# Performance work log

Hardware: AMD Instinct MI355X
Metric: run time of the kernel (lower is better)

The kernel has to match this reference:

```python
import jax, jax.numpy as jnp
import numpy as np

N, E = 50000, 1600000
IN_DIM, HID, HEADS, DH, NCLS = 1280, 256, 4, 64, 6
NEG_SLOPE = 0.2
LN_EPS = 1e-5


def setup_inputs() -> dict:
    key = jax.random.key(0)
    ks = jax.random.split(key, 24)
    p = {}
    p['x'] = jax.random.normal(ks[0], (N, IN_DIM), dtype=jnp.float32)
    p['edge_index'] = jax.random.randint(ks[1], (2, E), 0, N, dtype=jnp.int64)
    s = 0.05
    p['W_in'] = jax.random.normal(ks[2], (IN_DIM, HID), dtype=jnp.float32) * s
    p['b_in'] = jnp.zeros((HID,), jnp.float32)
    for l in range(2):
        p[f'W_gat{l}'] = jax.random.normal(ks[3 + 6 * l], (HID, HEADS * DH), dtype=jnp.float32) * s
        p[f'att_src{l}'] = jax.random.normal(ks[4 + 6 * l], (HEADS, DH), dtype=jnp.float32) * s
        p[f'att_dst{l}'] = jax.random.normal(ks[5 + 6 * l], (HEADS, DH), dtype=jnp.float32) * s
        p[f'b_gat{l}'] = jnp.zeros((HEADS * DH,), jnp.float32)
        p[f'ln_g{l}'] = jnp.ones((HID,), jnp.float32)
        p[f'ln_b{l}'] = jnp.zeros((HID,), jnp.float32)
    p['W_c1'] = jax.random.normal(ks[20], (HID, HID // 2), dtype=jnp.float32) * s
    p['b_c1'] = jnp.zeros((HID // 2,), jnp.float32)
    p['W_c2'] = jax.random.normal(ks[21], (HID // 2, NCLS), dtype=jnp.float32) * s
    p['b_c2'] = jnp.zeros((NCLS,), jnp.float32)
    return p


def _layer_norm(h, g, b):
    mu = jnp.mean(h, axis=-1, keepdims=True)
    var = jnp.mean((h - mu) ** 2, axis=-1, keepdims=True)
    return (h - mu) * jax.lax.rsqrt(var + LN_EPS) * g + b


def _gat_conv(h, src, dst, W, a_src, a_dst, bias):
    # h: [N, HID] -> per-head projections [N, H, DH]
    xh = (h @ W).reshape(N, HEADS, DH)
    al_src = jnp.sum(xh * a_src, axis=-1)  # [N, H]
    al_dst = jnp.sum(xh * a_dst, axis=-1)  # [N, H]
    e = jax.nn.leaky_relu(al_src[src] + al_dst[dst], NEG_SLOPE)  # [E', H]
    # edge softmax over incoming edges of each destination node
    m = jax.ops.segment_max(e, dst, num_segments=N)
    e = jnp.exp(e - m[dst])
    denom = jax.ops.segment_sum(e, dst, num_segments=N)
    w = e / denom[dst]  # [E', H]
    msg = xh[src] * w[:, :, None]  # [E', H, DH]
    out = jax.ops.segment_sum(msg, dst, num_segments=N)  # [N, H, DH]
    return out.reshape(N, HEADS * DH) + bias


def reference(x, edge_index, W_in, b_in, W_gat0, att_src0, att_dst0, b_gat0, ln_g0, ln_b0,
              W_gat1, att_src1, att_dst1, b_gat1, ln_g1, ln_b1, W_c1, b_c1, W_c2, b_c2):
    # add self loops (PyG GATConv default)
    loop = jnp.arange(N, dtype=edge_index.dtype)
    src = jnp.concatenate([edge_index[0], loop])
    dst = jnp.concatenate([edge_index[1], loop])

    h = jax.nn.relu(x @ W_in + b_in)

    for (Wg, asrc, adst, bg, g, b) in ((W_gat0, att_src0, att_dst0, b_gat0, ln_g0, ln_b0),
                                       (W_gat1, att_src1, att_dst1, b_gat1, ln_g1, ln_b1)):
        h_new = _gat_conv(h, src, dst, Wg, asrc, adst, bg)
        h_new = jax.nn.relu(_layer_norm(h_new, g, b))
        h = h + h_new

    logits = jax.nn.relu(h @ W_c1 + b_c1) @ W_c2 + b_c2
    return logits
```

## Files before the change

### kernel.cpp

```cpp
#include <hip/hip_runtime.h>

#define NN 50000
#define EE 1600000
#define INDIM 1280
#define HID 256
#define HEADS 4
#define DHD 64
#define NCLS 6
#define NEG 0.2f
#define LNEPS 1e-5f

typedef __attribute__((ext_vector_type(8))) short short8;
typedef __attribute__((ext_vector_type(4))) float floatx4;

__device__ __forceinline__ unsigned short f2b(float f) {
    unsigned int u = __float_as_uint(f);
    u += 0x7FFF + ((u >> 16) & 1);
    return (unsigned short)(u >> 16);
}
__device__ __forceinline__ float b2f(unsigned short b) {
    return __uint_as_float(((unsigned int)b) << 16);
}

#define WAIT_LGKM0() __builtin_amdgcn_s_waitcnt(0xC07F)
#define VMCNT6() asm volatile("s_waitcnt vmcnt(6)" ::: "memory")
#define VMCNT0() asm volatile("s_waitcnt vmcnt(0)" ::: "memory")

typedef const __attribute__((address_space(1))) unsigned int g_u32;
typedef __attribute__((address_space(3))) unsigned int l_u32;
#define GLOAD16(gp, lp) __builtin_amdgcn_global_load_lds((g_u32*)(gp), (l_u32*)(lp), 16, 0, 0)

__global__ void init_cnt_kernel(int* __restrict__ cnt) {
    int n = blockIdx.x * 256 + threadIdx.x;
    if (n < NN) cnt[n] = 1;
}

__global__ void count_edges_kernel(const int* __restrict__ dst, int* __restrict__ cnt) {
    int e = blockIdx.x * 256 + threadIdx.x;
    if (e < EE) atomicAdd(&cnt[dst[e]], 1);
}

__global__ __launch_bounds__(1024) void scan1_kernel(const int* __restrict__ cnt,
                                                     int* __restrict__ scanned,
                                                     int* __restrict__ chtot, int n) {
    __shared__ int wsum[16];
    int tid = threadIdx.x, lane = tid & 63, wv = tid >> 6;
    int i = blockIdx.x * 1024 + tid;
    int s = (i < n) ? cnt[i] : 0;
#pragma unroll
    for (int off = 1; off < 64; off <<= 1) {
        int t = __shfl_up(s, off, 64);
        if (lane >= off) s += t;
    }
    if (lane == 63) wsum[wv] = s;
    __syncthreads();
    if (tid < 16) {
        int ws = wsum[tid];
#pragma unroll
        for (int off = 1; off < 16; off <<= 1) {
            int t = __shfl_up(ws, off, 16);
            if (tid >= off) ws += t;
        }
        wsum[tid] = ws;
    }
    __syncthreads();
    s += (wv > 0) ? wsum[wv - 1] : 0;
    if (i < n) scanned[i] = s;
    if (tid == 1023) chtot[blockIdx.x] = s;
}

__global__ void scan2_kernel(int* __restrict__ chtot, int nch) {
    int lane = threadIdx.x;
    int v = (lane < nch) ? chtot[lane] : 0;
#pragma unroll
    for (int off = 1; off < 64; off <<= 1) {
        int t = __shfl_up(v, off, 64);
        if (lane >= off) v += t;
    }
    if (lane < nch) chtot[lane] = v;
}

__global__ void scan3_kernel(const int* __restrict__ scanned, const int* __restrict__ chtot,
                             int* __restrict__ rowptr, int n) {
    int i = blockIdx.x * 256 + threadIdx.x;
    if (i == 0) rowptr[0] = 0;
    if (i < n) {
        int ch = i >> 10;
        rowptr[i + 1] = scanned[i] + (ch ? chtot[ch - 1] : 0);
    }
}

__global__ void copyfill_kernel(const int* __restrict__ rowptr, int* __restrict__ cursor,
                                int* __restrict__ csr) {
    int n = blockIdx.x * 256 + threadIdx.x;
    if (n < NN) {
        int p = rowptr[n];
        csr[p] = n;
        cursor[n] = p + 1;
    }
}

__global__ void scatter_edges_kernel(const int* __restrict__ src, const int* __restrict__ dst,
                                     int* __restrict__ cursor, int* __restrict__ csr) {
    int e = blockIdx.x * 256 + threadIdx.x;
    if (e < EE) {
        int d = dst[e];
        int pos = atomicAdd(&cursor[d], 1);
        csr[pos] = src[e];
    }
}

__global__ void pack_w_kernel(const float* __restrict__ W, unsigned short* __restrict__ out,
                              int K, int N) {
    int idx = blockIdx.x * 256 + threadIdx.x;
    int total = (K >> 6) * (N >> 4) * 2 * 64;
    if (idx >= total) return;
    int ln = idx & 63;
    int t = idx >> 6;
    int ks = t & 1; t >>= 1;
    int NT = N >> 4;
    int nt = t % NT, kc = t / NT;
    int n = nt * 16 + (ln & 15);
    int k = kc * 64 + ks * 32 + ((ln >> 4) << 3);
    unsigned short u[8];
#pragma unroll
    for (int j = 0; j < 8; j++) u[j] = f2b(W[(size_t)(k + j) * N + n]);
    *(int4*)&out[(size_t)idx * 8] = *(const int4*)u;
}

__global__ void pack_w32_kernel(const float* __restrict__ W, unsigned short* __restrict__ out) {
    int idx = blockIdx.x * 256 + threadIdx.x;
    if (idx >= 40 * 16 * 64) return;
    int ln = idx & 63;
    int t = idx >> 6;
    int nt = t & 15;
    int s = t >> 4;
    int n = nt * 16 + (ln & 15);
    int k = s * 32 + ((ln >> 4) << 3);
    unsigned short u[8];
#pragma unroll
    for (int j = 0; j < 8; j++) u[j] = f2b(W[(size_t)(k + j) * HID + n]);
    *(int4*)&out[(size_t)idx * 8] = *(const int4*)u;
}

__global__ __launch_bounds__(256) void inproj_kernel(const float* __restrict__ Af,
                                                     const unsigned short* __restrict__ B32,
                                                     const float* __restrict__ bias,
                                                     float* __restrict__ Cf,
                                                     unsigned short* __restrict__ Cb) {
    constexpr int KS = 40;
    constexpr int ABYTES = 8192;
    constexpr int BBYTES = 16384;
    constexpr int SBYTES = ABYTES + BBYTES;
    __shared__ __align__(16) char lds[3 * SBYTES];
    int tid = threadIdx.x, wv = tid >> 6, ln = tid & 63;
    int m0 = blockIdx.x * 64;

    int arow0 = wv * 16 + (ln >> 3);
    int arow1 = arow0 + 8;
    int acb = ((ln & 7) * 16) ^ (((ln >> 3) & 7) << 4);
    const char* asrc0 = (const char*)(Af + (size_t)min(m0 + arow0, NN - 1) * INDIM) + acb;
    const char* asrc1 = (const char*)(Af + (size_t)min(m0 + arow1, NN - 1) * INDIM) + acb;
    const char* bsrc = (const char*)B32 + wv * 4096 + ln * 16;

    int aslot = wv * 2048 + ln * 16;
    int bslot = wv * 4096 + ln * 16;

    auto issue = [&](int k) {
        char* a = &lds[(k % 3) * SBYTES];
        char* b = a + ABYTES;
        GLOAD16(asrc0 + (size_t)k * 128, a + aslot);
        GLOAD16(asrc1 + (size_t)k * 128, a + aslot + 1024);
        const char* bs = bsrc + (size_t)k * BBYTES;
        GLOAD16(bs, b + bslot);
        GLOAD16(bs + 1024, b + bslot + 1024);
        GLOAD16(bs + 2048, b + bslot + 2048);
        GLOAD16(bs + 3072, b + bslot + 3072);
    };

    floatx4 acc[4][4] = {};
    int g32 = (ln >> 4) * 32;

    issue(0);
    issue(1);

    for (int k = 0; k < KS; k++) {
        if (k == KS - 1) VMCNT0(); else VMCNT6();
        __builtin_amdgcn_s_barrier();
        asm volatile("" ::: "memory");
        if (k + 2 < KS) issue(k + 2);

        const char* a = &lds[(k % 3) * SBYTES];
        const char* b = a + ABYTES;
        short8 bfrag[4];
#pragma unroll
        for (int nw = 0; nw < 4; nw++)
            bfrag[nw] = *(const short8*)(b + (((wv * 4 + nw) * 64 + ln) << 4));
#pragma unroll
        for (int mt = 0; mt < 4; mt++) {
            int row = mt * 16 + (ln & 15);
            int base = row * 128;
            int sw = (row & 7) << 4;
            float4 f0 = *(const float4*)(a + base + (g32 ^ sw));
            float4 f1 = *(const float4*)(a + base + ((g32 + 16) ^ sw));
            union { int4 i; short8 s; } u;
            asm("v_cvt_pk_bf16_f32 %0, %1, %2" : "=v"(u.i.x) : "v"(f0.x), "v"(f0.y));
            asm("v_cvt_pk_bf16_f32 %0, %1, %2" : "=v"(u.i.y) : "v"(f0.z), "v"(f0.w));
            asm("v_cvt_pk_bf16_f32 %0, %1, %2" : "=v"(u.i.z) : "v"(f1.x), "v"(f1.y));
            asm("v_cvt_pk_bf16_f32 %0, %1, %2" : "=v"(u.i.w) : "v"(f1.z), "v"(f1.w));
#pragma unroll
            for (int nw = 0; nw < 4; nw++)
                acc[mt][nw] = __builtin_amdgcn_mfma_f32_16x16x32_bf16(
                    u.s, bfrag[nw], acc[mt][nw], 0, 0, 0);
        }
        asm volatile("" ::: "memory");
    }

#pragma unroll
    for (int mt = 0; mt < 4; mt++) {
#pragma unroll
        for (int nw = 0; nw < 4; nw++) {
            int col = (wv * 4 + nw) * 16 + (ln & 15);
            int rb = m0 + mt * 16 + (ln >> 4) * 4;
            float bi = bias[col];
#pragma unroll
            for (int r = 0; r < 4; r++) {
                int row = rb + r;
                if (row < NN) {
                    float v = fmaxf(acc[mt][nw][r] + bi, 0.f);
                    Cf[(size_t)row * HID + col] = v;
                    Cb[(size_t)row * HID + col] = f2b(v);
                }
            }
        }
    }
}

template <int KI, int NT, int ACT, int WB16, int PROJ, int CLS>
__global__ __launch_bounds__(256) void pgemm_kernel(const unsigned short* __restrict__ Ab,
                                                    const unsigned short* __restrict__ Bf,
                                                    const float* __restrict__ bias,
                                                    unsigned short* __restrict__ Cb,
                                                    const float* __restrict__ aps,
                                                    const float* __restrict__ apd,
                                                    float* __restrict__ als,
                                                    float* __restrict__ ald,
                                                    const float* __restrict__ W2,
                                                    const float* __restrict__ b2,
                                                    float* __restrict__ out2,
                                                    int M) {
    constexpr int NW = NT / 4;
    constexpr int K = KI * 64;
    __shared__ __align__(16) unsigned short Als[2][4096];
    int tid = threadIdx.x, wv = tid >> 6, ln = tid & 63;
    int m0 = blockIdx.x * 64;

    int srow[2], scol[2];
#pragma unroll
    for (int i = 0; i < 2; i++) {
        int s = tid + i * 256;
        int r = s >> 3;
        srow[i] = min(m0 + r, M - 1);
        scol[i] = ((s & 7) ^ (r & 7)) * 8;
    }

    floatx4 acc[4][NW] = {};
    short8 breg[2][NW * 2];
    int4 ai0[2], ai1[2];

    auto issueA = [&](int k, int4* ai) {
#pragma unroll
        for (int i = 0; i < 2; i++)
            ai[i] = *(const int4*)(Ab + (size_t)srow[i] * K + k * 64 + scol[i]);
    };
    auto issueB = [&](int k, short8* b) {
#pragma unroll
        for (int nw = 0; nw < NW; nw++)
#pragma unroll
            for (int ks = 0; ks < 2; ks++)
                b[nw * 2 + ks] = *(const short8*)(
                    Bf + ((((size_t)k * NT + (wv * NW + nw)) * 2 + ks) * 64 + ln) * 8);
    };
    auto writeA = [&](int k, const int4* ai) {
        unsigned short* dst = &Als[k & 1][0];
#pragma unroll
        for (int i = 0; i < 2; i++) *(int4*)&dst[(tid + i * 256) * 8] = ai[i];
    };
    auto compute = [&](int k, const short8* b) {
        const unsigned short* src = &Als[k & 1][0];
#pragma unroll
        for (int ks = 0; ks < 2; ks++) {
            short8 a[4];
#pragma unroll
            for (int mt = 0; mt < 4; mt++) {
                int row = mt * 16 + (ln & 15);
                int g = ks * 4 + (ln >> 4);
                a[mt] = *(const short8*)&src[row * 64 + (g ^ (row & 7)) * 8];
            }
#pragma unroll
            for (int nw = 0; nw < NW; nw++)
#pragma unroll
                for (int mt = 0; mt < 4; mt++)
                    acc[mt][nw] = __builtin_amdgcn_mfma_f32_16x16x32_bf16(
                        a[mt], b[nw * 2 + ks], acc[mt][nw], 0, 0, 0);
        }
    };

    issueA(0, ai0);
    issueB(0, breg[0]);
    writeA(0, ai0);
    WAIT_LGKM0();
    __builtin_amdgcn_s_barrier();

#pragma unroll
    for (int kk = 0; kk < KI / 2; kk++) {
        int k = kk * 2;
        issueA(k + 1, ai1);
        issueB(k + 1, breg[1]);
        compute(k, breg[0]);
        writeA(k + 1, ai1);
        WAIT_LGKM0();
        __builtin_amdgcn_s_barrier();
        if (k + 2 < KI) {
            issueA(k + 2, ai0);
            issueB(k + 2, breg[0]);
        }
        compute(k + 1, breg[1]);
        if (k + 2 < KI) {
            writeA(k + 2, ai0);
            WAIT_LGKM0();
            __builtin_amdgcn_s_barrier();
        }
    }

    constexpr int Nout = NT * 16;
    if constexpr (WB16) {
#pragma unroll
        for (int mt = 0; mt < 4; mt++) {
#pragma unroll
            for (int nw = 0; nw < NW; nw++) {
                int col = (wv * NW + nw) * 16 + (ln & 15);
                int rb = m0 + mt * 16 + (ln >> 4) * 4;
                float bi = bias ? bias[col] : 0.f;
#pragma unroll
                for (int r = 0; r < 4; r++) {
                    int row = rb + r;
                    if (row < M) {
                        float v = acc[mt][nw][r] + bi;
                        if (ACT) v = fmaxf(v, 0.f);
                        Cb[(size_t)row * Nout + col] = f2b(v);
                    }
                }
            }
        }
    }

    if constexpr (PROJ) {
        float avs[NW], avd[NW];
#pragma unroll
        for (int nw = 0; nw < NW; nw++) {
            int d = nw * 16 + (ln & 15);
            avs[nw] = aps[wv * DHD + d];
            avd[nw] = apd[wv * DHD + d];
        }
#pragma unroll
        for (int mt = 0; mt < 4; mt++) {
#pragma unroll
            for (int r = 0; r < 4; r++) {
                float ssum = 0.f, dsum = 0.f;
#pragma unroll
                for (int nw = 0; nw < NW; nw++) {
                    float v = acc[mt][nw][r];
                    ssum = fmaf(v, avs[nw], ssum);
                    dsum = fmaf(v, avd[nw], dsum);
                }
#pragma unroll
                for (int m = 8; m > 0; m >>= 1) {
                    ssum += __shfl_xor(ssum, m, 16);
                    dsum += __shfl_xor(dsum, m, 16);
                }
                int row = m0 + mt * 16 + (ln >> 4) * 4 + r;
                if ((ln & 15) == 0 && row < M) {
                    als[row * 4 + wv] = ssum;
                    ald[row * 4 + wv] = dsum;
                }
            }
        }
    }

    if constexpr (CLS) {
        __shared__ float cred[64][4][NCLS];
        float w2[NW][NCLS];
#pragma unroll
        for (int nw = 0; nw < NW; nw++) {
            int col = (wv * NW + nw) * 16 + (ln & 15);
#pragma unroll
            for (int c = 0; c < NCLS; c++) w2[nw][c] = W2[col * NCLS + c];
        }
#pragma unroll
        for (int mt = 0; mt < 4; mt++) {
#pragma unroll
            for (int r = 0; r < 4; r++) {
                float p[NCLS] = {};
#pragma unroll
                for (int nw = 0; nw < NW; nw++) {
                    int col = (wv * NW + nw) * 16 + (ln & 15);
                    float v = fmaxf(acc[mt][nw][r] + bias[col], 0.f);
#pragma unroll
                    for (int c = 0; c < NCLS; c++) p[c] = fmaf(v, w2[nw][c], p[c]);
                }
#pragma unroll
                for (int m = 8; m > 0; m >>= 1)
#pragma unroll
                    for (int c = 0; c < NCLS; c++) p[c] += __shfl_xor(p[c], m, 16);
                int rl = mt * 16 + (ln >> 4) * 4 + r;
                if ((ln & 15) == 0)
#pragma unroll
                    for (int c = 0; c < NCLS; c++) cred[rl][wv][c] = p[c];
            }
        }
        __syncthreads();
        for (int t = tid; t < 64 * NCLS; t += 256) {
            int row = t / NCLS, c = t % NCLS;
            if (m0 + row < M) {
                float s = cred[row][0][c] + cred[row][1][c] + cred[row][2][c] +
                          cred[row][3][c] + b2[c];
                out2[(size_t)(m0 + row) * NCLS + c] = s;
            }
        }
    }
}

__global__ __launch_bounds__(256) void agg_ln_kernel(const int* __restrict__ rowptr,
                                                     const int* __restrict__ csr,
                                                     const float* __restrict__ al_s,
                                                     const float* __restrict__ al_d,
                                                     const unsigned short* __restrict__ xhb,
                                                     const float* __restrict__ bgat,
                                                     const float* __restrict__ g,
                                                     const float* __restrict__ bb,
                                                     float* __restrict__ h,
                                                     unsigned short* __restrict__ hb) {
    int wv = threadIdx.x >> 6, ln = threadIdx.x & 63;
    int n = blockIdx.x * 4 + wv;
    if (n >= NN) return;
    int start = rowptr[n], end = rowptr[n + 1];
    int half = ln >> 5;
    int j = ln & 31;
    int head = j >> 3;
    float adh = al_d[n * 4 + head];

    float p[8] = {}, q[8] = {};
    float dsp = 0.f, dsq = 0.f;

    int i = start + half;
    for (; i + 2 < end; i += 4) {
        int s0 = csr[i], s1 = csr[i + 2];
        float e0 = al_s[s0 * 4 + head] + adh; e0 = e0 > 0.f ? e0 : NEG * e0;
        float e1 = al_s[s1 * 4 + head] + adh; e1 = e1 > 0.f ? e1 : NEG * e1;
        float w0 = __expf(e0), w1 = __expf(e1);
        dsp += w0; dsq += w1;
        short8 u0 = *(const short8*)&xhb[(size_t)s0 * HID + j * 8];
        short8 u1 = *(const short8*)&xhb[(size_t)s1 * HID + j * 8];
#pragma unroll
        for (int k = 0; k < 8; k++) {
            p[k] = fmaf(w0, b2f((unsigned short)u0[k]), p[k]);
            q[k] = fmaf(w1, b2f((unsigned short)u1[k]), q[k]);
        }
    }
    if (i < end) {
        int s0 = csr[i];
        float e0 = al_s[s0 * 4 + head] + adh; e0 = e0 > 0.f ? e0 : NEG * e0;
        float w0 = __expf(e0);
        dsp += w0;
        short8 u0 = *(const short8*)&xhb[(size_t)s0 * HID + j * 8];
#pragma unroll
        for (int k = 0; k < 8; k++) p[k] = fmaf(w0, b2f((unsigned short)u0[k]), p[k]);
    }

    float ds = dsp + dsq;
    ds += __shfl_xor(ds, 32, 64);
    float inv = 1.f / ds;

    const float4* bgp = (const float4*)&bgat[j * 8];
    float4 bg0 = bgp[0], bg1 = bgp[1];
    float bgk[8] = {bg0.x, bg0.y, bg0.z, bg0.w, bg1.x, bg1.y, bg1.z, bg1.w};

    float vv[8];
    float ps = 0.f, ps2 = 0.f;
#pragma unroll
    for (int k = 0; k < 8; k++) {
        float t = p[k] + q[k];
        t += __shfl_xor(t, 32, 64);
        float val = t * inv + bgk[k];
        vv[k] = val;
        ps += val;
        ps2 = fmaf(val, val, ps2);
    }
#pragma unroll
    for (int off = 16; off > 0; off >>= 1) {
        ps += __shfl_xor(ps, off, 64);
        ps2 += __shfl_xor(ps2, off, 64);
    }
    float mu = ps * (1.f / HID);
    float var = ps2 * (1.f / HID) - mu * mu;
    float rs = rsqrtf(var + LNEPS);

    const float4* gp = (const float4*)&g[j * 8];
    const float4* bp = (const float4*)&bb[j * 8];
    float4 g0 = gp[0], g1 = gp[1];
    float4 c0 = bp[0], c1 = bp[1];
    float gk[8] = {g0.x, g0.y, g0.z, g0.w, g1.x, g1.y, g1.z, g1.w};
    float ck[8] = {c0.x, c0.y, c0.z, c0.w, c1.x, c1.y, c1.z, c1.w};

    size_t idx = (size_t)n * HID + j * 8;
    const float4* hp = (const float4*)&h[idx];
    float4 h0 = hp[0], h1 = hp[1];
    float hk[8] = {h0.x, h0.y, h0.z, h0.w, h1.x, h1.y, h1.z, h1.w};

    float nh[8];
#pragma unroll
    for (int k = 0; k < 8; k++) {
        float o = fmaxf((vv[k] - mu) * rs * gk[k] + ck[k], 0.f);
        nh[k] = hk[k] + o;
    }

    if (half == 0) {
        ((float4*)&h[idx])[0] = make_float4(nh[0], nh[1], nh[2], nh[3]);
        ((float4*)&h[idx])[1] = make_float4(nh[4], nh[5], nh[6], nh[7]);
    } else {
        unsigned short ub[8];
#pragma unroll
        for (int k = 0; k < 8; k++) ub[k] = f2b(nh[k]);
        *(int4*)&hb[idx] = *(const int4*)ub;
    }
}

extern "C" void kernel_launch(void* const* d_in, const int* in_sizes, int n_in,
                              void* d_out, int out_size, void* d_ws, size_t ws_size,
                              hipStream_t stream) {
    const float* x    = (const float*)d_in[0];
    const int*   ei   = (const int*)d_in[1];
    const float* W_in = (const float*)d_in[2];
    const float* b_in = (const float*)d_in[3];
    const float* W_gat[2]   = {(const float*)d_in[4],  (const float*)d_in[10]};
    const float* att_src[2] = {(const float*)d_in[5],  (const float*)d_in[11]};
    const float* att_dst[2] = {(const float*)d_in[6],  (const float*)d_in[12]};
    const float* b_gat[2]   = {(const float*)d_in[7],  (const float*)d_in[13]};
    const float* ln_g[2]    = {(const float*)d_in[8],  (const float*)d_in[14]};
    const float* ln_b[2]    = {(const float*)d_in[9],  (const float*)d_in[15]};
    const float* W_c1 = (const float*)d_in[16];
    const float* b_c1 = (const float*)d_in[17];
    const float* W_c2 = (const float*)d_in[18];
    const float* b_c2 = (const float*)d_in[19];

    char* ws = (char*)d_ws;
    size_t off = 0;
    auto alloc = [&](size_t bytes) -> void* {
        void* p = ws + off;
        off += (bytes + 255) & ~(size_t)255;
        return p;
    };
    float*          h   = (float*)alloc((size_t)NN * HID * 4);
    unsigned short* hb  = (unsigned short*)alloc((size_t)NN * HID * 2);
    unsigned short* xhb = (unsigned short*)alloc((size_t)NN * HID * 2);
    float* al_s = (float*)alloc((size_t)NN * HEADS * 4);
    float* al_d = (float*)alloc((size_t)NN * HEADS * 4);
    int* rowptr  = (int*)alloc((size_t)(NN + 1) * 4);
    int* cursor  = (int*)alloc((size_t)NN * 4);
    int* csr     = (int*)alloc((size_t)(EE + NN) * 4);
    int* scanned = (int*)alloc((size_t)NN * 4);
    int* chtot   = (int*)alloc(64 * 4);
    unsigned short* Win32 = (unsigned short*)alloc((size_t)HID * INDIM * 2);
    unsigned short* WgF0 = (unsigned short*)alloc((size_t)HID * HID * 2);
    unsigned short* WgF1 = (unsigned short*)alloc((size_t)HID * HID * 2);
    unsigned short* Wc1F = (unsigned short*)alloc((size_t)(HID / 2) * HID * 2);
    unsigned short* WgF[2] = {WgF0, WgF1};

    const int* srcv = ei;
    const int* dstv = ei + EE;

    pack_w32_kernel<<<(40 * 16 * 64 + 255) / 256, 256, 0, stream>>>(W_in, Win32);
    pack_w_kernel<<<(HID * HID / 8 + 255) / 256, 256, 0, stream>>>(W_gat[0], WgF0, HID, HID);
    pack_w_kernel<<<(HID * HID / 8 + 255) / 256, 256, 0, stream>>>(W_gat[1], WgF1, HID, HID);
    pack_w_kernel<<<(HID * (HID / 2) / 8 + 255) / 256, 256, 0, stream>>>(W_c1, Wc1F, HID, HID / 2);

    int nch = (NN + 1023) / 1024;
    init_cnt_kernel<<<(NN + 255) / 256, 256, 0, stream>>>(cursor);
    count_edges_kernel<<<(EE + 255) / 256, 256, 0, stream>>>(dstv, cursor);
    scan1_kernel<<<nch, 1024, 0, stream>>>(cursor, scanned, chtot, NN);
    scan2_kernel<<<1, 64, 0, stream>>>(chtot, nch);
    scan3_kernel<<<(NN + 255) / 256, 256, 0, stream>>>(scanned, chtot, rowptr, NN);
    copyfill_kernel<<<(NN + 255) / 256, 256, 0, stream>>>(rowptr, cursor, csr);
    scatter_edges_kernel<<<(EE + 255) / 256, 256, 0, stream>>>(srcv, dstv, cursor, csr);

    inproj_kernel<<<(NN + 63) / 64, 256, 0, stream>>>(x, Win32, b_in, h, hb);

    int MB64 = (NN + 63) / 64;
    for (int l = 0; l < 2; l++) {
        pgemm_kernel<4, 16, 0, 1, 1, 0><<<MB64, 256, 0, stream>>>(
            hb, WgF[l], nullptr, xhb,
            att_src[l], att_dst[l], al_s, al_d, nullptr, nullptr, nullptr, NN);
        agg_ln_kernel<<<(NN + 3) / 4, 256, 0, stream>>>(rowptr, csr, al_s, al_d, xhb,
                                                        b_gat[l], ln_g[l], ln_b[l], h, hb);
    }

    pgemm_kernel<4, 8, 1, 0, 0, 1><<<MB64, 256, 0, stream>>>(
        hb, Wc1F, b_c1, nullptr,
        nullptr, nullptr, nullptr, nullptr, W_c2, b_c2, (float*)d_out, NN);
}
```

Measured before the change: 998.0 us.

## Merge weight packing kernels, fold scan2 into scan3, unroll aggregation loop deeper

The four weight-packing launches become one kernel that dispatches on the flat index. The chunk-total scan is recomputed per block inside scan3 through shared memory, which removes a separate launch. The GAT aggregation loop now handles four edges per half-wave per iteration instead of two, so more gathers are in flight, and a loop replaces the single-edge tail. Together these cut launch overhead and raise memory-level parallelism, at the cost of higher register pressure in the aggregation kernel.

New measurement: 993.7 us. No clear change (-0.4%).

```diff
diff --git a/kernel.cpp b/kernel.cpp
--- a/kernel.cpp
+++ b/kernel.cpp
@@ -69,24 +69,25 @@
     if (tid == 1023) chtot[blockIdx.x] = s;
 }
 
-__global__ void scan2_kernel(int* __restrict__ chtot, int nch) {
-    int lane = threadIdx.x;
-    int v = (lane < nch) ? chtot[lane] : 0;
-#pragma unroll
-    for (int off = 1; off < 64; off <<= 1) {
-        int t = __shfl_up(v, off, 64);
-        if (lane >= off) v += t;
-    }
-    if (lane < nch) chtot[lane] = v;
-}
-
 __global__ void scan3_kernel(const int* __restrict__ scanned, const int* __restrict__ chtot,
-                             int* __restrict__ rowptr, int n) {
-    int i = blockIdx.x * 256 + threadIdx.x;
+                             int* __restrict__ rowptr, int n, int nch) {
+    __shared__ int pre[64];
+    int tid = threadIdx.x;
+    if (tid < 64) {
+        int v = (tid < nch) ? chtot[tid] : 0;
+#pragma unroll
+        for (int off = 1; off < 64; off <<= 1) {
+            int t = __shfl_up(v, off, 64);
+            if (tid >= off) v += t;
+        }
+        pre[tid] = v;
+    }
+    __syncthreads();
+    int i = blockIdx.x * 256 + tid;
     if (i == 0) rowptr[0] = 0;
     if (i < n) {
         int ch = i >> 10;
-        rowptr[i + 1] = scanned[i] + (ch ? chtot[ch - 1] : 0);
+        rowptr[i + 1] = scanned[i] + (ch ? pre[ch - 1] : 0);
     }
 }
 
@@ -110,11 +111,9 @@
     }
 }
 
-__global__ void pack_w_kernel(const float* __restrict__ W, unsigned short* __restrict__ out,
-                              int K, int N) {
-    int idx = blockIdx.x * 256 + threadIdx.x;
-    int total = (K >> 6) * (N >> 4) * 2 * 64;
-    if (idx >= total) return;
+__device__ __forceinline__ void pack_frag(const float* __restrict__ W,
+                                          unsigned short* __restrict__ out,
+                                          int K, int N, int idx) {
     int ln = idx & 63;
     int t = idx >> 6;
     int ks = t & 1; t >>= 1;
@@ -128,19 +127,33 @@
     *(int4*)&out[(size_t)idx * 8] = *(const int4*)u;
 }
 
-__global__ void pack_w32_kernel(const float* __restrict__ W, unsigned short* __restrict__ out) {
+__global__ void pack_all_kernel(const float* __restrict__ Win, unsigned short* __restrict__ Win32,
+                                const float* __restrict__ Wg0, unsigned short* __restrict__ WgF0,
+                                const float* __restrict__ Wg1, unsigned short* __restrict__ WgF1,
+                                const float* __restrict__ Wc1, unsigned short* __restrict__ Wc1F) {
     int idx = blockIdx.x * 256 + threadIdx.x;
-    if (idx >= 40 * 16 * 64) return;
-    int ln = idx & 63;
-    int t = idx >> 6;
-    int nt = t & 15;
-    int s = t >> 4;
-    int n = nt * 16 + (ln & 15);
-    int k = s * 32 + ((ln >> 4) << 3);
-    unsigned short u[8];
-#pragma unroll
-    for (int j = 0; j < 8; j++) u[j] = f2b(W[(size_t)(k + j) * HID + n]);
-    *(int4*)&out[(size_t)idx * 8] = *(const int4*)u;
+    const int S0 = 40 * 16 * 64;
+    const int S1 = (HID >> 6) * (HID >> 4) * 2 * 64;
+    const int S3 = (HID >> 6) * ((HID / 2) >> 4) * 2 * 64;
+    if (idx < S0) {
+        int ln = idx & 63;
+        int t = idx >> 6;
+        int nt = t & 15;
+        int s = t >> 4;
+        int n = nt * 16 + (ln & 15);
+        int k = s * 32 + ((ln >> 4) << 3);
+        unsigned short u[8];
+#pragma unroll
+        for (int j = 0; j < 8; j++) u[j] = f2b(Win[(size_t)(k + j) * HID + n]);
+        *(int4*)&Win32[(size_t)idx * 8] = *(const int4*)u;
+        return;
+    }
+    idx -= S0;
+    if (idx < S1) { pack_frag(Wg0, WgF0, HID, HID, idx); return; }
+    idx -= S1;
+    if (idx < S1) { pack_frag(Wg1, WgF1, HID, HID, idx); return; }
+    idx -= S1;
+    if (idx < S3) pack_frag(Wc1, Wc1F, HID, HID / 2, idx);
 }
 
 __global__ __launch_bounds__(256) void inproj_kernel(const float* __restrict__ Af,
@@ -454,21 +467,31 @@
     float dsp = 0.f, dsq = 0.f;
 
     int i = start + half;
-    for (; i + 2 < end; i += 4) {
-        int s0 = csr[i], s1 = csr[i + 2];
+    for (; i + 6 < end; i += 8) {
+        int s0 = csr[i], s1 = csr[i + 2], s2 = csr[i + 4], s3 = csr[i + 6];
         float e0 = al_s[s0 * 4 + head] + adh; e0 = e0 > 0.f ? e0 : NEG * e0;
         float e1 = al_s[s1 * 4 + head] + adh; e1 = e1 > 0.f ? e1 : NEG * e1;
-        float w0 = __expf(e0), w1 = __expf(e1);
-        dsp += w0; dsq += w1;
+        float e2 = al_s[s2 * 4 + head] + adh; e2 = e2 > 0.f ? e2 : NEG * e2;
+        float e3 = al_s[s3 * 4 + head] + adh; e3 = e3 > 0.f ? e3 : NEG * e3;
+        float w0 = __expf(e0), w1 = __expf(e1), w2 = __expf(e2), w3 = __expf(e3);
         short8 u0 = *(const short8*)&xhb[(size_t)s0 * HID + j * 8];
         short8 u1 = *(const short8*)&xhb[(size_t)s1 * HID + j * 8];
+        short8 u2 = *(const short8*)&xhb[(size_t)s2 * HID + j * 8];
+        short8 u3 = *(const short8*)&xhb[(size_t)s3 * HID + j * 8];
+        dsp += w0 + w2;
+        dsq += w1 + w3;
 #pragma unroll
         for (int k = 0; k < 8; k++) {
             p[k] = fmaf(w0, b2f((unsigned short)u0[k]), p[k]);
             q[k] = fmaf(w1, b2f((unsigned short)u1[k]), q[k]);
         }
-    }
-    if (i < end) {
+#pragma unroll
+        for (int k = 0; k < 8; k++) {
+            p[k] = fmaf(w2, b2f((unsigned short)u2[k]), p[k]);
+            q[k] = fmaf(w3, b2f((unsigned short)u3[k]), q[k]);
+        }
+    }
+    for (; i < end; i += 2) {
         int s0 = csr[i];
         float e0 = al_s[s0 * 4 + head] + adh; e0 = e0 > 0.f ? e0 : NEG * e0;
         float w0 = __expf(e0);
@@ -580,17 +603,14 @@
     const int* srcv = ei;
     const int* dstv = ei + EE;
 
-    pack_w32_kernel<<<(40 * 16 * 64 + 255) / 256, 256, 0, stream>>>(W_in, Win32);
-    pack_w_kernel<<<(HID * HID / 8 + 255) / 256, 256, 0, stream>>>(W_gat[0], WgF0, HID, HID);
-    pack_w_kernel<<<(HID * HID / 8 + 255) / 256, 256, 0, stream>>>(W_gat[1], WgF1, HID, HID);
-    pack_w_kernel<<<(HID * (HID / 2) / 8 + 255) / 256, 256, 0, stream>>>(W_c1, Wc1F, HID, HID / 2);
+    pack_all_kernel<<<240, 256, 0, stream>>>(W_in, Win32, W_gat[0], WgF0,
+                                             W_gat[1], WgF1, W_c1, Wc1F);
 
     int nch = (NN + 1023) / 1024;
     init_cnt_kernel<<<(NN + 255) / 256, 256, 0, stream>>>(cursor);
     count_edges_kernel<<<(EE + 255) / 256, 256, 0, stream>>>(dstv, cursor);
     scan1_kernel<<<nch, 1024, 0, stream>>>(cursor, scanned, chtot, NN);
-    scan2_kernel<<<1, 64, 0, stream>>>(chtot, nch);
-    scan3_kernel<<<(NN + 255) / 256, 256, 0, stream>>>(scanned, chtot, rowptr, NN);
+    scan3_kernel<<<(NN + 255) / 256, 256, 0, stream>>>(scanned, chtot, rowptr, NN, nch);
     copyfill_kernel<<<(NN + 255) / 256, 256, 0, stream>>>(rowptr, cursor, csr);
     scatter_edges_kernel<<<(EE + 255) / 256, 256, 0, stream>>>(srcv, dstv, cursor, csr);
 
```
